# Kernel tuning notes

Measured on AMD Instinct MI355X. Metric: run time of the kernel, lower is better.

Reference implementation:

```python
import jax, jax.numpy as jnp
import numpy as np

B, C_IN, N, K, S, C_OUT = 256, 8, 4096, 9, 2, 8

def setup_inputs() -> dict:
    key = jax.random.key(0)
    k1, k2, k3, k4, k5 = jax.random.split(key, 5)
    scale = (1.0 / (C_IN * K)) ** 0.5  # matches uniform(-sqrt(k), sqrt(k)) magnitude
    x = jax.random.normal(k1, (B, C_IN, N), dtype=jnp.float32)
    neighborhoods = jax.random.randint(k2, (N, K), 0, N, dtype=jnp.int32)
    sub_ids = jax.random.randint(k3, (N,), 0, S, dtype=jnp.int32)
    weight = jax.random.uniform(k4, (S, C_IN, K, C_OUT), dtype=jnp.float32, minval=-scale, maxval=scale)
    bias = jax.random.uniform(k5, (S, C_OUT), dtype=jnp.float32, minval=-scale, maxval=scale)
    return {"x": x, "neighborhoods": neighborhoods, "sub_ids": sub_ids, "weight": weight, "bias": bias}

def reference(x, neighborhoods, sub_ids, weight, bias):
    # x: [B, C_in, N]; neighborhoods: [N, K]; sub_ids: [N]
    # weight: [S, C_in, K, C_out]; bias: [S, C_out]
    rel = x[:, :, neighborhoods]            # [B, C_in, N, K]  (per-site neighbor gather)
    w_site = weight[sub_ids]                # [N, C_in, K, C_out] (per-site sublattice weight)
    out = jnp.einsum('bcnk,nckd->bdn', rel, w_site)  # [B, C_out, N]
    out = out + bias[sub_ids].T[None]       # broadcast [1, C_out, N]
    return out
```

## Files before the change

### kernel.cpp

```cpp
#include <hip/hip_runtime.h>
#include <stdint.h>
#include <stddef.h>

#define BSZ  256
#define NSZ  4096
#define CIN  8
#define KNB  9
#define DOUT 8
#define NSUB 2

typedef __fp16   fh2  __attribute__((ext_vector_type(2)));
typedef float    f2   __attribute__((ext_vector_type(2)));
typedef float    f4   __attribute__((ext_vector_type(4)));
typedef int      i2   __attribute__((ext_vector_type(2)));
typedef uint32_t u32x4 __attribute__((ext_vector_type(4)));

static __device__ __forceinline__ uint32_t pk_f16(float a, float b) {
    fh2 h = __builtin_amdgcn_cvt_pkrtz(a, b);
    return __builtin_bit_cast(uint32_t, h);
}

static __device__ __forceinline__ float dot2(uint32_t a, uint32_t b, float c) {
#if __has_builtin(__builtin_amdgcn_fdot2)
    return __builtin_amdgcn_fdot2(__builtin_bit_cast(fh2, a),
                                  __builtin_bit_cast(fh2, b), c, false);
#else
    fh2 x = __builtin_bit_cast(fh2, a), y = __builtin_bit_cast(fh2, b);
    return c + (float)x[0] * (float)y[0] + (float)x[1] * (float)y[1];
#endif
}

__global__ void pack_w_kernel(const float* __restrict__ w, uint32_t* __restrict__ wp) {
    int i = threadIdx.x;
    if (i >= NSUB * KNB * 4 * DOUT) return;
    int d = i & 7, cp = (i >> 3) & 3, r = i >> 5;
    int k = r % KNB, s = r / KNB;
    float w0 = w[((s * CIN + 2 * cp    ) * KNB + k) * DOUT + d];
    float w1 = w[((s * CIN + 2 * cp + 1) * KNB + k) * DOUT + d];
    wp[i] = pk_f16(w0, w1);
}

__global__ __launch_bounds__(1024) void latconv_kernel(
    const float* __restrict__ x, const int* __restrict__ nbh,
    const int* __restrict__ sub, const uint32_t* __restrict__ wp,
    const float* __restrict__ bias, float* __restrict__ out)
{
    __shared__ __align__(16) uint32_t xl[NSZ * 4];

    const int b    = blockIdx.x & 255;
    const int half = blockIdx.x >> 8;
    const int t    = threadIdx.x;
    const float* xb = x + (size_t)b * (CIN * NSZ);

    {
        const int j0 = 4 * t;
        f4 v[CIN];
        #pragma unroll
        for (int c = 0; c < CIN; ++c)
            v[c] = *reinterpret_cast<const f4*>(xb + c * NSZ + j0);
        #pragma unroll
        for (int jj = 0; jj < 4; ++jj) {
            u32x4 row;
            #pragma unroll
            for (int cp = 0; cp < 4; ++cp)
                row[cp] = pk_f16(v[2 * cp][jj], v[2 * cp + 1][jj]);
            *reinterpret_cast<u32x4*>(&xl[(size_t)(j0 + jj) * 4]) = row;
        }
    }

    float bias0[DOUT], bias1[DOUT];
    #pragma unroll
    for (int d = 0; d < DOUT; ++d) { bias0[d] = bias[d]; bias1[d] = bias[DOUT + d]; }

    const int n0 = 2 * t + 2048 * half;

    const i2 s2 = *reinterpret_cast<const i2*>(sub + n0);
    const int sv[2] = { s2[0], s2[1] };

    uint32_t ja[2][KNB];
    {
        i2 q[KNB];
        const i2* np2 = reinterpret_cast<const i2*>(nbh + (size_t)n0 * KNB);
        #pragma unroll
        for (int r = 0; r < KNB; ++r) q[r] = np2[r];
        const int* qs = reinterpret_cast<const int*>(q);
        #pragma unroll
        for (int i = 0; i < 2; ++i)
            #pragma unroll
            for (int k = 0; k < KNB; ++k)
                ja[i][k] = (uint32_t)qs[i * KNB + k] << 4;
    }

    float acc[2][DOUT];
    #pragma unroll
    for (int i = 0; i < 2; ++i)
        #pragma unroll
        for (int d = 0; d < DOUT; ++d)
            acc[i][d] = sv[i] ? bias1[d] : bias0[d];

    __syncthreads();

    const char* xlb = reinterpret_cast<const char*>(xl);
    for (int k = 0; k < KNB; ++k) {
        u32x4 xv[2];
        #pragma unroll
        for (int i = 0; i < 2; ++i)
            xv[i] = *reinterpret_cast<const u32x4*>(xlb + ja[i][k]);
        #pragma unroll
        for (int cp = 0; cp < 4; ++cp) {
            const uint32_t* w0p = wp + ((0 * KNB + k) * 4 + cp) * 8;
            const uint32_t* w1p = wp + ((1 * KNB + k) * 4 + cp) * 8;
            uint32_t wq0[DOUT], wq1[DOUT];
            #pragma unroll
            for (int d = 0; d < DOUT; ++d) { wq0[d] = w0p[d]; wq1[d] = w1p[d]; }
            #pragma unroll
            for (int i = 0; i < 2; ++i) {
                #pragma unroll
                for (int d = 0; d < DOUT; ++d) {
                    const uint32_t wsel = sv[i] ? wq1[d] : wq0[d];
                    acc[i][d] = dot2(xv[i][cp], wsel, acc[i][d]);
                }
            }
        }
    }

    #pragma unroll
    for (int d = 0; d < DOUT; ++d) {
        f2 o = { acc[0][d], acc[1][d] };
        *reinterpret_cast<f2*>(out + ((size_t)b * DOUT + d) * NSZ + n0) = o;
    }
}

extern "C" void kernel_launch(void* const* d_in, const int* in_sizes, int n_in,
                              void* d_out, int out_size, void* d_ws, size_t ws_size,
                              hipStream_t stream) {
    const float* x    = (const float*)d_in[0];
    const int*   nbh  = (const int*)d_in[1];
    const int*   sub  = (const int*)d_in[2];
    const float* w    = (const float*)d_in[3];
    const float* bias = (const float*)d_in[4];
    float* out = (float*)d_out;
    uint32_t* wp = (uint32_t*)d_ws;

    pack_w_kernel<<<1, 576, 0, stream>>>(w, wp);
    latconv_kernel<<<2 * BSZ, 1024, 0, stream>>>(x, nbh, sub, wp, bias, out);
}
```

Before: 120.9 us.

## Compute lattice convolution with MFMA 16x16x32 f16 instead of dot2 loops

```diff
diff --git a/kernel.cpp b/kernel.cpp
--- a/kernel.cpp
+++ b/kernel.cpp
@@ -10,9 +10,8 @@
 #define NSUB 2
 
 typedef __fp16   fh2  __attribute__((ext_vector_type(2)));
-typedef float    f2   __attribute__((ext_vector_type(2)));
+typedef __fp16   v8fh __attribute__((ext_vector_type(8)));
 typedef float    f4   __attribute__((ext_vector_type(4)));
-typedef int      i2   __attribute__((ext_vector_type(2)));
 typedef uint32_t u32x4 __attribute__((ext_vector_type(4)));
 
 static __device__ __forceinline__ uint32_t pk_f16(float a, float b) {
@@ -20,32 +19,30 @@
     return __builtin_bit_cast(uint32_t, h);
 }
 
-static __device__ __forceinline__ float dot2(uint32_t a, uint32_t b, float c) {
-#if __has_builtin(__builtin_amdgcn_fdot2)
-    return __builtin_amdgcn_fdot2(__builtin_bit_cast(fh2, a),
-                                  __builtin_bit_cast(fh2, b), c, false);
-#else
-    fh2 x = __builtin_bit_cast(fh2, a), y = __builtin_bit_cast(fh2, b);
-    return c + (float)x[0] * (float)y[0] + (float)x[1] * (float)y[1];
-#endif
-}
-
-__global__ void pack_w_kernel(const float* __restrict__ w, uint32_t* __restrict__ wp) {
-    int i = threadIdx.x;
-    if (i >= NSUB * KNB * 4 * DOUT) return;
-    int d = i & 7, cp = (i >> 3) & 3, r = i >> 5;
-    int k = r % KNB, s = r / KNB;
-    float w0 = w[((s * CIN + 2 * cp    ) * KNB + k) * DOUT + d];
-    float w1 = w[((s * CIN + 2 * cp + 1) * KNB + k) * DOUT + d];
-    wp[i] = pk_f16(w0, w1);
+__global__ void pack_bfrag_kernel(const float* __restrict__ w, uint32_t* __restrict__ btab) {
+    int t = threadIdx.x;
+    if (t >= NSUB * 3 * 64) return;
+    int lane = t & 63, s = (t >> 6) % 3, sg = t / 192;
+    int g = lane >> 4, d = lane & 15, ks = s * 4 + g;
+    u32x4 row;
+    #pragma unroll
+    for (int cp = 0; cp < 4; ++cp) {
+        float v0 = 0.f, v1 = 0.f;
+        if (d < DOUT && ks < KNB) {
+            v0 = w[((sg * CIN + 2 * cp    ) * KNB + ks) * DOUT + d];
+            v1 = w[((sg * CIN + 2 * cp + 1) * KNB + ks) * DOUT + d];
+        }
+        row[cp] = pk_f16(v0, v1);
+    }
+    reinterpret_cast<u32x4*>(btab)[t] = row;
 }
 
 __global__ __launch_bounds__(1024) void latconv_kernel(
     const float* __restrict__ x, const int* __restrict__ nbh,
-    const int* __restrict__ sub, const uint32_t* __restrict__ wp,
+    const int* __restrict__ sub, const uint32_t* __restrict__ btab,
     const float* __restrict__ bias, float* __restrict__ out)
 {
-    __shared__ __align__(16) uint32_t xl[NSZ * 4];
+    __shared__ __align__(16) uint32_t xl[(NSZ + 1) * 4];
 
     const int b    = blockIdx.x & 255;
     const int half = blockIdx.x >> 8;
@@ -67,67 +64,60 @@
             *reinterpret_cast<u32x4*>(&xl[(size_t)(j0 + jj) * 4]) = row;
         }
     }
-
-    float bias0[DOUT], bias1[DOUT];
-    #pragma unroll
-    for (int d = 0; d < DOUT; ++d) { bias0[d] = bias[d]; bias1[d] = bias[DOUT + d]; }
-
-    const int n0 = 2 * t + 2048 * half;
-
-    const i2 s2 = *reinterpret_cast<const i2*>(sub + n0);
-    const int sv[2] = { s2[0], s2[1] };
-
-    uint32_t ja[2][KNB];
-    {
-        i2 q[KNB];
-        const i2* np2 = reinterpret_cast<const i2*>(nbh + (size_t)n0 * KNB);
-        #pragma unroll
-        for (int r = 0; r < KNB; ++r) q[r] = np2[r];
-        const int* qs = reinterpret_cast<const int*>(q);
-        #pragma unroll
-        for (int i = 0; i < 2; ++i)
-            #pragma unroll
-            for (int k = 0; k < KNB; ++k)
-                ja[i][k] = (uint32_t)qs[i * KNB + k] << 4;
+    if (t == 0) {
+        u32x4 z = { 0, 0, 0, 0 };
+        *reinterpret_cast<u32x4*>(&xl[(size_t)NSZ * 4]) = z;
     }
 
-    float acc[2][DOUT];
+    const int lane = t & 63, wv = t >> 6;
+    const int g = lane >> 4, r = lane & 15, d = r;
+
+    u32x4 bf[2][3];
     #pragma unroll
-    for (int i = 0; i < 2; ++i)
+    for (int sg = 0; sg < 2; ++sg)
         #pragma unroll
-        for (int d = 0; d < DOUT; ++d)
-            acc[i][d] = sv[i] ? bias1[d] : bias0[d];
+        for (int s = 0; s < 3; ++s)
+            bf[sg][s] = reinterpret_cast<const u32x4*>(btab)[(sg * 3 + s) * 64 + lane];
+
+    const float bz0 = bias[d & 7];
+    const float bz1 = bias[DOUT + (d & 7)];
 
     __syncthreads();
 
     const char* xlb = reinterpret_cast<const char*>(xl);
-    for (int k = 0; k < KNB; ++k) {
-        u32x4 xv[2];
+    #pragma unroll 2
+    for (int tile = 0; tile < 8; ++tile) {
+        const int n0 = half * 2048 + wv * 128 + tile * 16;
+
+        const int4 sv = *reinterpret_cast<const int4*>(sub + n0 + g * 4);
+
+        int js[3];
         #pragma unroll
-        for (int i = 0; i < 2; ++i)
-            xv[i] = *reinterpret_cast<const u32x4*>(xlb + ja[i][k]);
+        for (int s = 0; s < 3; ++s) {
+            const int ks = s * 4 + g;
+            js[s] = (ks < KNB) ? nbh[(n0 + r) * KNB + ks] : NSZ;
+        }
+
+        f4 a0 = { 0.f, 0.f, 0.f, 0.f };
+        f4 a1 = { 0.f, 0.f, 0.f, 0.f };
         #pragma unroll
-        for (int cp = 0; cp < 4; ++cp) {
-            const uint32_t* w0p = wp + ((0 * KNB + k) * 4 + cp) * 8;
-            const uint32_t* w1p = wp + ((1 * KNB + k) * 4 + cp) * 8;
-            uint32_t wq0[DOUT], wq1[DOUT];
+        for (int s = 0; s < 3; ++s) {
+            const u32x4 av = *reinterpret_cast<const u32x4*>(xlb + ((size_t)(uint32_t)js[s] << 4));
+            const v8fh af = __builtin_bit_cast(v8fh, av);
+            a0 = __builtin_amdgcn_mfma_f32_16x16x32_f16(af, __builtin_bit_cast(v8fh, bf[0][s]), a0, 0, 0, 0);
+            a1 = __builtin_amdgcn_mfma_f32_16x16x32_f16(af, __builtin_bit_cast(v8fh, bf[1][s]), a1, 0, 0, 0);
+        }
+
+        if (d < DOUT) {
+            const int svv[4] = { sv.x, sv.y, sv.z, sv.w };
+            f4 o;
             #pragma unroll
-            for (int d = 0; d < DOUT; ++d) { wq0[d] = w0p[d]; wq1[d] = w1p[d]; }
-            #pragma unroll
-            for (int i = 0; i < 2; ++i) {
-                #pragma unroll
-                for (int d = 0; d < DOUT; ++d) {
-                    const uint32_t wsel = sv[i] ? wq1[d] : wq0[d];
-                    acc[i][d] = dot2(xv[i][cp], wsel, acc[i][d]);
-                }
+            for (int reg = 0; reg < 4; ++reg) {
+                const float acc = svv[reg] ? a1[reg] : a0[reg];
+                o[reg] = acc + (svv[reg] ? bz1 : bz0);
             }
+            *reinterpret_cast<f4*>(out + ((size_t)b * DOUT + d) * NSZ + n0 + g * 4) = o;
         }
-    }
-
-    #pragma unroll
-    for (int d = 0; d < DOUT; ++d) {
-        f2 o = { acc[0][d], acc[1][d] };
-        *reinterpret_cast<f2*>(out + ((size_t)b * DOUT + d) * NSZ + n0) = o;
     }
 }
 
@@ -140,8 +130,8 @@
     const float* w    = (const float*)d_in[3];
     const float* bias = (const float*)d_in[4];
     float* out = (float*)d_out;
-    uint32_t* wp = (uint32_t*)d_ws;
+    uint32_t* btab = (uint32_t*)d_ws;
 
-    pack_w_kernel<<<1, 576, 0, stream>>>(w, wp);
-    latconv_kernel<<<2 * BSZ, 1024, 0, stream>>>(x, nbh, sub, wp, bias, out);
+    pack_bfrag_kernel<<<1, 384, 0, stream>>>(w, btab);
+    latconv_kernel<<<2 * BSZ, 1024, 0, stream>>>(x, nbh, sub, btab, bias, out);
 }
```

Result: faster. 105.8 us (-12.5%).
